# Kernel optimization log

Hardware: AMD Instinct MI355X
Metric: run time of the kernel (lower is better)

Reference implementation:

```python
import jax, jax.numpy as jnp
import numpy as np

MAX_PATH_DISTANCE = 5

def setup_inputs() -> dict:
    key = jax.random.key(0)
    k1, k2, k3, k4, k5 = jax.random.split(key, 5)
    N = 8192
    E = 8_000_000
    x = jax.random.normal(k1, (N, 128), dtype=jnp.float32)
    src = jax.random.randint(k2, (E,), 0, N, dtype=jnp.int32)
    dst = jax.random.randint(k3, (E,), 0, N, dtype=jnp.int32)
    # path lengths >= 1 (a path always contains at least the source node)
    path_len = jax.random.randint(k4, (E,), 1, 11, dtype=jnp.int32)
    b = jax.random.normal(k5, (MAX_PATH_DISTANCE,), dtype=jnp.float32)
    return {"x": x, "src": src, "dst": dst, "path_len": path_len, "b": b}

def reference(x, src, dst, path_len, b):
    N = x.shape[0]
    # bias index: min(len, max_path_distance) - 1, clamped to valid range
    idx = jnp.clip(path_len, 1, MAX_PATH_DISTANCE) - 1
    vals = b[idx]                                  # [E] gather from small bias vector
    spatial = jnp.zeros((N, N), dtype=b.dtype)
    spatial = spatial.at[src, dst].set(vals)       # scatter into dense NxN matrix
    return spatial
```

## Files before the change

kernel.cpp:

```cpp
#include <hip/hip_runtime.h>


constexpr int MAXPD      = 5;
constexpr int NROW       = 8192;
constexpr int SLAB_ROWS  = 32;
constexpr int NSLAB      = NROW / SLAB_ROWS;
constexpr int SLOTS_ROW  = NROW / 2;
constexpr int STRIDE     = 9 * SLOTS_ROW;
constexpr int PAIR_CAP   = SLOTS_ROW;
constexpr int CHUNK      = 4096;
constexpr int CUR_PAD    = 16;
constexpr int E_MAX      = 8388606;

__device__ __forceinline__ long long slab_slot(unsigned int s, unsigned int i) {
    unsigned int row = s * 32u + 1u + 2u * (i >> 12);
    return (long long)row * SLOTS_ROW + (i & 4095u);
}

__device__ __forceinline__ float dec(unsigned int k, float b0, float b1,
                                     float b2, float b3, float b4) {
    if (k == 0u) return 0.0f;
    unsigned int bi = k & 7u;
    float v = b0;
    v = (bi == 1u) ? b1 : v;
    v = (bi == 2u) ? b2 : v;
    v = (bi == 3u) ? b3 : v;
    v = (bi == 4u) ? b4 : v;
    return v;
}

__global__ void zero_ws_kernel(unsigned int* __restrict__ w, int n) {
    int i = blockIdx.x * blockDim.x + threadIdx.x;
    if (i < n) w[i] = 0u;
}


__global__ __launch_bounds__(256) void stage1_bin(
        const int* __restrict__ gsrc, const int* __restrict__ gdst,
        const int* __restrict__ gpl, unsigned long long* __restrict__ out64,
        unsigned int* __restrict__ slabcur, int E) {
    __shared__ unsigned long long sorted[CHUNK];
    __shared__ unsigned int hist[NSLAB];
    __shared__ unsigned int offs[NSLAB];
    __shared__ unsigned int cur2[NSLAB];
    __shared__ unsigned int gbase[NSLAB];
    __shared__ unsigned int wsum[4];

    const int t = threadIdx.x;
    const int base = blockIdx.x * CHUNK;
    const int cnt = min(CHUNK, E - base);

    hist[t] = 0u;
    __syncthreads();

    unsigned long long rec[16];

    #pragma unroll
    for (int k = 0; k < 4; ++k) {
        int g = base + (k * 256 + t) * 4;
        bool full = (g + 3 < E);
        int4 s4 = {0,0,0,0}, d4 = {0,0,0,0}, p4 = {1,1,1,1};
        if (full) {
            s4 = ((const int4*)gsrc)[g >> 2];
            d4 = ((const int4*)gdst)[g >> 2];
            p4 = ((const int4*)gpl)[g >> 2];
        }
        #pragma unroll
        for (int j = 0; j < 4; ++j) {
            int e = g + j;
            unsigned long long r = 0ull;
            if (full || e < E) {
                int ss, dd, pp;
                if (full) {
                    ss = (j == 0) ? s4.x : (j == 1) ? s4.y : (j == 2) ? s4.z : s4.w;
                    dd = (j == 0) ? d4.x : (j == 1) ? d4.y : (j == 2) ? d4.z : d4.w;
                    pp = (j == 0) ? p4.x : (j == 1) ? p4.y : (j == 2) ? p4.z : p4.w;
                } else {
                    ss = gsrc[e]; dd = gdst[e]; pp = gpl[e];
                }
                int bi = pp < 1 ? 0 : (pp > MAXPD ? MAXPD - 1 : pp - 1);
                unsigned int key = (((unsigned int)e + 1u) << 3) | (unsigned int)bi;
                r = ((unsigned long long)key << 26) |
                    ((unsigned long long)(unsigned int)ss << 13) |
                    (unsigned long long)(unsigned int)dd;
                atomicAdd(&hist[(unsigned int)ss >> 5], 1u);
            }
            rec[k * 4 + j] = r;
        }
    }
    __syncthreads();

    unsigned int h = hist[t];
    unsigned int incl = h;
    #pragma unroll
    for (int d = 1; d < 64; d <<= 1) {
        unsigned int v = __shfl_up(incl, d, 64);
        if ((t & 63) >= d) incl += v;
    }
    int wv = t >> 6;
    if ((t & 63) == 63) wsum[wv] = incl;
    __syncthreads();
    unsigned int wpre = 0;
    for (int w = 0; w < wv; ++w) wpre += wsum[w];
    unsigned int excl = wpre + incl - h;
    offs[t] = excl;
    cur2[t] = excl;
    if (h) gbase[t] = atomicAdd(&slabcur[t * CUR_PAD], h);
    __syncthreads();

    #pragma unroll
    for (int m = 0; m < 16; ++m) {
        unsigned long long r = rec[m];
        if (r) {
            unsigned int slab = (unsigned int)(r >> 18) & 255u;
            unsigned int p = atomicAdd(&cur2[slab], 1u);
            sorted[p] = r;
        }
    }
    __syncthreads();

    for (int i = t; i < cnt; i += 256) {
        unsigned long long r = sorted[i];
        unsigned int slab = (unsigned int)(r >> 18) & 255u;
        unsigned int pos = gbase[slab] + ((unsigned int)i - offs[slab]);
        if (pos < (unsigned int)STRIDE) out64[slab_slot(slab, pos)] = r;
    }
}


__global__ __launch_bounds__(1024) void stage2_rebin(
        unsigned long long* __restrict__ out64,
        const unsigned int* __restrict__ slabcur,
        unsigned int* __restrict__ paircnt) {
    __shared__ unsigned int pcur[16];
    const int s = blockIdx.x, t = threadIdx.x;
    if (t < 16) pcur[t] = 0u;
    __syncthreads();
    unsigned int cnt = slabcur[s * CUR_PAD];
    if (cnt > (unsigned int)STRIDE) cnt = STRIDE;
    for (unsigned int i = t; i < cnt; i += 1024) {
        unsigned long long r = out64[slab_slot(s, i)];
        unsigned int q = ((unsigned int)(r >> 14)) & 15u;
        unsigned int pos = atomicAdd(&pcur[q], 1u);
        if (pos < (unsigned int)PAIR_CAP) {
            unsigned int row = (unsigned int)s * 32u + 2u * q;
            out64[(long long)row * SLOTS_ROW + pos] = r;
        }
    }
    __syncthreads();
    if (t < 16) {
        unsigned int c = pcur[t];
        paircnt[s * 16 + t] = (c > (unsigned int)PAIR_CAP) ? (unsigned int)PAIR_CAP : c;
    }
}


__global__ __launch_bounds__(512) void stage3_resolve(
        unsigned int* __restrict__ out32,
        const unsigned int* __restrict__ paircnt,
        const float* __restrict__ b) {
    __shared__ unsigned int tab[2 * NROW];
    const int p = blockIdx.x, t = threadIdx.x;
    uint4* t4 = (uint4*)tab;
    #pragma unroll
    for (int j = 0; j < 8; ++j) t4[t + j * 512] = make_uint4(0u, 0u, 0u, 0u);
    __syncthreads();

    unsigned int cnt = paircnt[p];
    const unsigned long long* list =
        (const unsigned long long*)out32 + (long long)(2 * p) * SLOTS_ROW;
    for (unsigned int i = t; i < cnt; i += 512) {
        unsigned long long r = list[i];
        unsigned int d  = (unsigned int)r & 8191u;
        unsigned int rl = ((unsigned int)(r >> 13)) & 1u;
        unsigned int key = (unsigned int)(r >> 26);
        atomicMax(&tab[rl * NROW + d], key);
    }
    __syncthreads();

    const float b0 = b[0], b1 = b[1], b2 = b[2], b3 = b[3], b4 = b[4];
    float4* orow = (float4*)(out32 + (long long)(2 * p) * NROW);
    #pragma unroll
    for (int j = 0; j < 8; ++j) {
        uint4 k = t4[t + j * 512];
        float4 v;
        v.x = dec(k.x, b0, b1, b2, b3, b4);
        v.y = dec(k.y, b0, b1, b2, b3, b4);
        v.z = dec(k.z, b0, b1, b2, b3, b4);
        v.w = dec(k.w, b0, b1, b2, b3, b4);
        orow[j * 512 + t] = v;
    }
}


__global__ void zero_keys_kernel(unsigned int* __restrict__ out, long long n) {
    long long n4 = n >> 2;
    long long i = (long long)blockIdx.x * blockDim.x + threadIdx.x;
    long long stride = (long long)gridDim.x * blockDim.x;
    uint4* p = reinterpret_cast<uint4*>(out);
    for (long long j = i; j < n4; j += stride) p[j] = make_uint4(0u, 0u, 0u, 0u);
    long long base = n4 << 2;
    for (long long j = base + i; j < n; j += stride) out[j] = 0u;
}

__global__ void scatter_keys_kernel(const int* __restrict__ src,
                                    const int* __restrict__ dst,
                                    const int* __restrict__ plen,
                                    unsigned int* __restrict__ keys,
                                    int E, int N) {
    int i = blockIdx.x * blockDim.x + threadIdx.x;
    int stride = gridDim.x * blockDim.x;
    for (int e = i; e < E; e += stride) {
        int s = src[e], d = dst[e], pl = plen[e];
        int bi = pl < 1 ? 0 : (pl > MAXPD ? MAXPD - 1 : pl - 1);
        unsigned int key = (((unsigned int)e + 1u) << 3) | (unsigned int)bi;
        atomicMax(keys + (long long)s * (long long)N + d, key);
    }
}

__global__ void decode_keys_kernel(unsigned int* __restrict__ data, long long n,
                                   const float* __restrict__ b) {
    __shared__ float sb[8];
    if (threadIdx.x < 8) sb[threadIdx.x] = (threadIdx.x < MAXPD) ? b[threadIdx.x] : 0.0f;
    __syncthreads();
    long long n4 = n >> 2;
    long long i = (long long)blockIdx.x * blockDim.x + threadIdx.x;
    long long stride = (long long)gridDim.x * blockDim.x;
    uint4* p = reinterpret_cast<uint4*>(data);
    float4* f = reinterpret_cast<float4*>(data);
    for (long long j = i; j < n4; j += stride) {
        uint4 k = p[j];
        float4 v;
        v.x = k.x ? sb[k.x & 7u] : 0.0f;
        v.y = k.y ? sb[k.y & 7u] : 0.0f;
        v.z = k.z ? sb[k.z & 7u] : 0.0f;
        v.w = k.w ? sb[k.w & 7u] : 0.0f;
        f[j] = v;
    }
    long long base = n4 << 2;
    float* fo = reinterpret_cast<float*>(data);
    for (long long j = base + i; j < n; j += stride) {
        unsigned int k = data[j];
        fo[j] = k ? sb[k & 7u] : 0.0f;
    }
}

extern "C" void kernel_launch(void* const* d_in, const int* in_sizes, int n_in,
                              void* d_out, int out_size, void* d_ws, size_t ws_size,
                              hipStream_t stream) {
    const int* src  = (const int*)d_in[1];
    const int* dst  = (const int*)d_in[2];
    const int* plen = (const int*)d_in[3];
    const float* b  = (const float*)d_in[4];

    int N = in_sizes[0] / 128;
    int E = in_sizes[1];
    long long n = (long long)out_size;

    const size_t ws_need = (size_t)(NSLAB * CUR_PAD + NSLAB * 16) * 4;

    if (N == NROW && n == (long long)NROW * NROW && E > 0 && E <= E_MAX &&
        ws_size >= ws_need) {
        unsigned int* slabcur = (unsigned int*)d_ws;
        unsigned int* paircnt = slabcur + NSLAB * CUR_PAD;
        unsigned long long* out64 = (unsigned long long*)d_out;
        unsigned int* out32 = (unsigned int*)d_out;

        int nzero = NSLAB * CUR_PAD;
        zero_ws_kernel<<<(nzero + 255) / 256, 256, 0, stream>>>(slabcur, nzero);

        int nchunk = (E + CHUNK - 1) / CHUNK;
        stage1_bin<<<nchunk, 256, 0, stream>>>(src, dst, plen, out64, slabcur, E);
        stage2_rebin<<<NSLAB, 1024, 0, stream>>>(out64, slabcur, paircnt);
        stage3_resolve<<<NROW / 2, 512, 0, stream>>>(out32, paircnt, b);
    } else {
        unsigned int* keys = (unsigned int*)d_out;
        const int BLK = 256;
        int grid_zero = (int)min((n / 4 + BLK - 1) / BLK, (long long)2048);
        int grid_scat = min((E + BLK - 1) / BLK, 2048);
        zero_keys_kernel<<<grid_zero, BLK, 0, stream>>>(keys, n);
        scatter_keys_kernel<<<grid_scat, BLK, 0, stream>>>(src, dst, plen, keys, E, N);
        decode_keys_kernel<<<grid_zero, BLK, 0, stream>>>(keys, n, b);
    }
}
```

Before: 168.9 us.

## Double stage1 chunk size, vectorize stage2/3 loads, use nontemporal output stores

Stage1 now runs 512 threads per block over 8192-edge chunks, which halves the number of per-block global slab atomics and histogram passes. Stages 2 and 3 read two 64-bit records per 16-byte load, with a tail case for odd counts. Stage3 runs 1024 threads and writes decoded rows with nontemporal stores so the final dense output bypasses cache. The bigger blocks raise shared memory and register pressure per block, which may reduce occupancy. The nontemporal stores may conflict with the in-place reuse of the output buffer as scratch space.

New measurement: 142.8 us. -15.4%, faster.

```diff
diff --git a/kernel.cpp b/kernel.cpp
--- a/kernel.cpp
+++ b/kernel.cpp
@@ -1,5 +1,7 @@
 #include <hip/hip_runtime.h>
 
+
+typedef float floatx4 __attribute__((ext_vector_type(4)));
 
 constexpr int MAXPD      = 5;
 constexpr int NROW       = 8192;
@@ -8,7 +10,7 @@
 constexpr int SLOTS_ROW  = NROW / 2;
 constexpr int STRIDE     = 9 * SLOTS_ROW;
 constexpr int PAIR_CAP   = SLOTS_ROW;
-constexpr int CHUNK      = 4096;
+constexpr int CHUNK      = 8192;
 constexpr int CUR_PAD    = 16;
 constexpr int E_MAX      = 8388606;
 
@@ -35,7 +37,7 @@
 }
 
 
-__global__ __launch_bounds__(256) void stage1_bin(
+__global__ __launch_bounds__(512) void stage1_bin(
         const int* __restrict__ gsrc, const int* __restrict__ gdst,
         const int* __restrict__ gpl, unsigned long long* __restrict__ out64,
         unsigned int* __restrict__ slabcur, int E) {
@@ -50,14 +52,14 @@
     const int base = blockIdx.x * CHUNK;
     const int cnt = min(CHUNK, E - base);
 
-    hist[t] = 0u;
+    if (t < NSLAB) hist[t] = 0u;
     __syncthreads();
 
     unsigned long long rec[16];
 
     #pragma unroll
     for (int k = 0; k < 4; ++k) {
-        int g = base + (k * 256 + t) * 4;
+        int g = base + (k * 512 + t) * 4;
         bool full = (g + 3 < E);
         int4 s4 = {0,0,0,0}, d4 = {0,0,0,0}, p4 = {1,1,1,1};
         if (full) {
@@ -90,22 +92,26 @@
     }
     __syncthreads();
 
-    unsigned int h = hist[t];
-    unsigned int incl = h;
-    #pragma unroll
-    for (int d = 1; d < 64; d <<= 1) {
-        unsigned int v = __shfl_up(incl, d, 64);
-        if ((t & 63) >= d) incl += v;
-    }
-    int wv = t >> 6;
-    if ((t & 63) == 63) wsum[wv] = incl;
-    __syncthreads();
-    unsigned int wpre = 0;
-    for (int w = 0; w < wv; ++w) wpre += wsum[w];
-    unsigned int excl = wpre + incl - h;
-    offs[t] = excl;
-    cur2[t] = excl;
-    if (h) gbase[t] = atomicAdd(&slabcur[t * CUR_PAD], h);
+    unsigned int h = 0, incl = 0;
+    if (t < NSLAB) {
+        h = hist[t];
+        incl = h;
+        #pragma unroll
+        for (int d = 1; d < 64; d <<= 1) {
+            unsigned int v = __shfl_up(incl, d, 64);
+            if ((t & 63) >= d) incl += v;
+        }
+        if ((t & 63) == 63) wsum[t >> 6] = incl;
+    }
+    __syncthreads();
+    if (t < NSLAB) {
+        unsigned int wpre = 0;
+        for (int w = 0; w < (t >> 6); ++w) wpre += wsum[w];
+        unsigned int excl = wpre + incl - h;
+        offs[t] = excl;
+        cur2[t] = excl;
+        gbase[t] = atomicAdd(&slabcur[t * CUR_PAD], h);
+    }
     __syncthreads();
 
     #pragma unroll
@@ -119,7 +125,7 @@
     }
     __syncthreads();
 
-    for (int i = t; i < cnt; i += 256) {
+    for (int i = t; i < cnt; i += 512) {
         unsigned long long r = sorted[i];
         unsigned int slab = (unsigned int)(r >> 18) & 255u;
         unsigned int pos = gbase[slab] + ((unsigned int)i - offs[slab]);
@@ -127,35 +133,51 @@
     }
 }
 
+
+__device__ __forceinline__ void s2_process(unsigned long long r,
+                                           unsigned int* pcur,
+                                           unsigned long long* out64,
+                                           unsigned int s) {
+    unsigned int q = ((unsigned int)(r >> 14)) & 15u;
+    unsigned int pos = atomicAdd(&pcur[q], 1u);
+    if (pos < (unsigned int)PAIR_CAP) {
+        unsigned int row = s * 32u + 2u * q;
+        out64[(long long)row * SLOTS_ROW + pos] = r;
+    }
+}
 
 __global__ __launch_bounds__(1024) void stage2_rebin(
         unsigned long long* __restrict__ out64,
         const unsigned int* __restrict__ slabcur,
         unsigned int* __restrict__ paircnt) {
     __shared__ unsigned int pcur[16];
-    const int s = blockIdx.x, t = threadIdx.x;
+    const unsigned int s = blockIdx.x;
+    const int t = threadIdx.x;
     if (t < 16) pcur[t] = 0u;
     __syncthreads();
     unsigned int cnt = slabcur[s * CUR_PAD];
     if (cnt > (unsigned int)STRIDE) cnt = STRIDE;
-    for (unsigned int i = t; i < cnt; i += 1024) {
-        unsigned long long r = out64[slab_slot(s, i)];
-        unsigned int q = ((unsigned int)(r >> 14)) & 15u;
-        unsigned int pos = atomicAdd(&pcur[q], 1u);
-        if (pos < (unsigned int)PAIR_CAP) {
-            unsigned int row = (unsigned int)s * 32u + 2u * q;
-            out64[(long long)row * SLOTS_ROW + pos] = r;
-        }
+    unsigned int cnt2 = cnt >> 1;
+    for (unsigned int i = t; i < cnt2; i += 1024) {
+        long long slot = slab_slot(s, 2u * i);
+        uint4 v = *reinterpret_cast<const uint4*>(&out64[slot]);
+        unsigned long long r0 = ((unsigned long long)v.y << 32) | v.x;
+        unsigned long long r1 = ((unsigned long long)v.w << 32) | v.z;
+        s2_process(r0, pcur, out64, s);
+        s2_process(r1, pcur, out64, s);
+    }
+    if (t == 0 && (cnt & 1u)) {
+        s2_process(out64[slab_slot(s, cnt - 1u)], pcur, out64, s);
     }
     __syncthreads();
     if (t < 16) {
         unsigned int c = pcur[t];
-        paircnt[s * 16 + t] = (c > (unsigned int)PAIR_CAP) ? (unsigned int)PAIR_CAP : c;
-    }
-}
-
-
-__global__ __launch_bounds__(512) void stage3_resolve(
+        paircnt[s * 16u + t] = (c > (unsigned int)PAIR_CAP) ? (unsigned int)PAIR_CAP : c;
+    }
+}
+
+
+__global__ __launch_bounds__(1024) void stage3_resolve(
         unsigned int* __restrict__ out32,
         const unsigned int* __restrict__ paircnt,
         const float* __restrict__ b) {
@@ -163,32 +185,43 @@
     const int p = blockIdx.x, t = threadIdx.x;
     uint4* t4 = (uint4*)tab;
     #pragma unroll
-    for (int j = 0; j < 8; ++j) t4[t + j * 512] = make_uint4(0u, 0u, 0u, 0u);
+    for (int j = 0; j < 4; ++j) t4[t + j * 1024] = make_uint4(0u, 0u, 0u, 0u);
     __syncthreads();
 
     unsigned int cnt = paircnt[p];
     const unsigned long long* list =
         (const unsigned long long*)out32 + (long long)(2 * p) * SLOTS_ROW;
-    for (unsigned int i = t; i < cnt; i += 512) {
-        unsigned long long r = list[i];
-        unsigned int d  = (unsigned int)r & 8191u;
-        unsigned int rl = ((unsigned int)(r >> 13)) & 1u;
-        unsigned int key = (unsigned int)(r >> 26);
-        atomicMax(&tab[rl * NROW + d], key);
+    unsigned int cnt2 = cnt >> 1;
+    for (unsigned int i = t; i < cnt2; i += 1024) {
+        uint4 v = reinterpret_cast<const uint4*>(list)[i];
+        unsigned long long r0 = ((unsigned long long)v.y << 32) | v.x;
+        unsigned long long r1 = ((unsigned long long)v.w << 32) | v.z;
+        atomicMax(&tab[(((unsigned int)(r0 >> 13)) & 1u) * NROW +
+                       ((unsigned int)r0 & 8191u)],
+                  (unsigned int)(r0 >> 26));
+        atomicMax(&tab[(((unsigned int)(r1 >> 13)) & 1u) * NROW +
+                       ((unsigned int)r1 & 8191u)],
+                  (unsigned int)(r1 >> 26));
+    }
+    if (t == 0 && (cnt & 1u)) {
+        unsigned long long r = list[cnt - 1u];
+        atomicMax(&tab[(((unsigned int)(r >> 13)) & 1u) * NROW +
+                       ((unsigned int)r & 8191u)],
+                  (unsigned int)(r >> 26));
     }
     __syncthreads();
 
     const float b0 = b[0], b1 = b[1], b2 = b[2], b3 = b[3], b4 = b[4];
-    float4* orow = (float4*)(out32 + (long long)(2 * p) * NROW);
+    floatx4* orow = reinterpret_cast<floatx4*>(out32 + (long long)(2 * p) * NROW);
     #pragma unroll
-    for (int j = 0; j < 8; ++j) {
-        uint4 k = t4[t + j * 512];
-        float4 v;
+    for (int j = 0; j < 4; ++j) {
+        uint4 k = t4[t + j * 1024];
+        floatx4 v;
         v.x = dec(k.x, b0, b1, b2, b3, b4);
         v.y = dec(k.y, b0, b1, b2, b3, b4);
         v.z = dec(k.z, b0, b1, b2, b3, b4);
         v.w = dec(k.w, b0, b1, b2, b3, b4);
-        orow[j * 512 + t] = v;
+        __builtin_nontemporal_store(v, &orow[j * 1024 + t]);
     }
 }
 
@@ -270,9 +303,9 @@
         zero_ws_kernel<<<(nzero + 255) / 256, 256, 0, stream>>>(slabcur, nzero);
 
         int nchunk = (E + CHUNK - 1) / CHUNK;
-        stage1_bin<<<nchunk, 256, 0, stream>>>(src, dst, plen, out64, slabcur, E);
+        stage1_bin<<<nchunk, 512, 0, stream>>>(src, dst, plen, out64, slabcur, E);
         stage2_rebin<<<NSLAB, 1024, 0, stream>>>(out64, slabcur, paircnt);
-        stage3_resolve<<<NROW / 2, 512, 0, stream>>>(out32, paircnt, b);
+        stage3_resolve<<<NROW / 2, 1024, 0, stream>>>(out32, paircnt, b);
     } else {
         unsigned int* keys = (unsigned int*)d_out;
         const int BLK = 256;
```
